# Kernel tuning notes

Hardware: AMD Instinct MI355X
Metric: run time of the kernel (lower is better)

Reference implementation:

```python
import jax, jax.numpy as jnp
import numpy as np

N_NODES = 50000
N_EDGES = 1600000
D_FEAT = 128
ORDER = 2


def setup_inputs() -> dict:
    key = jax.random.key(0)
    k1, k2, k3, k4 = jax.random.split(key, 4)
    x = jax.random.normal(k1, (N_NODES, D_FEAT), dtype=jnp.float32)
    adj_row = jax.random.randint(k2, (N_EDGES,), 0, N_NODES, dtype=jnp.int32)
    adj_col = jax.random.randint(k3, (N_EDGES,), 0, N_NODES, dtype=jnp.int32)
    adj_vals = jax.random.uniform(k4, (N_EDGES,), dtype=jnp.float32)
    return {"x": x, "adj_row": adj_row, "adj_col": adj_col, "adj_vals": adj_vals}


def reference(x, adj_row, adj_col, adj_vals):
    # SGC propagation: x <- A @ x, repeated `order` times.
    # A is sparse COO: A[row, col] = vals; spmm(A, x)[i] = sum_e vals[e]*x[col[e]] into row[e].
    for _ in range(ORDER):
        msgs = adj_vals[:, None] * x[adj_col]          # [E, F] gathered messages
        x = jax.ops.segment_sum(msgs, adj_row, num_segments=N_NODES)  # [N, F]
    return x
```

## Files before the change

kernel.cpp:

```cpp
#include <hip/hip_runtime.h>
#include <hip/hip_fp16.h>

#define N_NODES 50000
#define N_EDGES 1600000
#define D_FEAT  128
#define NB      196
#define BCAP    8704
#define SPAIR_STRIDE (BCAP * 2)
#define S_OUT_CAP 9216
#define OVF_CAP  8192
#define NWAVES  (N_NODES / 2)
#define XWORDS  (N_NODES * (D_FEAT / 2))

#define P1_WGS   400
#define P1_ROUND 4096
#define P1_CAP   38

typedef unsigned u32x2 __attribute__((ext_vector_type(2)));
typedef int      i32x4 __attribute__((ext_vector_type(4)));
typedef float    f32x2 __attribute__((ext_vector_type(2)));
typedef float    f32x4 __attribute__((ext_vector_type(4)));

__device__ __forceinline__ unsigned short f2bf(float f) {
    union { float f; unsigned u; } v; v.f = f;
    unsigned r = v.u + 0x7fff + ((v.u >> 16) & 1);
    return (unsigned short)(r >> 16);
}
__device__ __forceinline__ float bf_lo(unsigned w) {
    union { unsigned u; float f; } v; v.u = w << 16; return v.f;
}
__device__ __forceinline__ float bf_hi(unsigned w) {
    union { unsigned u; float f; } v; v.u = w & 0xffff0000u; return v.f;
}

__global__ __launch_bounds__(256) void p1_bin_kernel(
    const int* __restrict__ row, const int* __restrict__ col,
    const float* __restrict__ val,
    int* __restrict__ gcnt, uint2* __restrict__ sedge, uint2* __restrict__ ovf)
{
    __shared__ uint2    s_buf[NB * P1_CAP];
    __shared__ unsigned s_cnt[NB];
    __shared__ int      s_base[NB];

    int wg = blockIdx.x, t = threadIdx.x;
    int e0 = (int)((long)wg * N_EDGES / P1_WGS);
    int e1 = (int)((long)(wg + 1) * N_EDGES / P1_WGS);

    for (int rbase = e0; rbase < e1; rbase += P1_ROUND) {
        int rend = rbase + P1_ROUND; if (rend > e1) rend = e1;
        for (int i = t; i < NB; i += 256) s_cnt[i] = 0;
        __syncthreads();
        for (int e = rbase + t; e < rend; e += 256) {
            int r = row[e];
            int b = r >> 8;
            uint2 rec;
            rec.x = ((unsigned)r << 16) | (unsigned)col[e];
            rec.y = __float_as_uint(val[e]);
            unsigned pos = atomicAdd(&s_cnt[b], 1u);
            if (pos < P1_CAP) {
                s_buf[b * P1_CAP + pos] = rec;
            } else {
                int p = atomicAdd(&gcnt[b], 1);
                if (p < BCAP) sedge[(long)b * BCAP + p] = rec;
                else {
                    int q = atomicAdd(&gcnt[NB], 1);
                    if (q < OVF_CAP) ovf[q] = rec;
                }
            }
        }
        __syncthreads();
        if (t < NB) {
            int c = (int)s_cnt[t]; if (c > P1_CAP) c = P1_CAP;
            s_base[t] = (c > 0) ? atomicAdd(&gcnt[t], c) : 0;
        }
        __syncthreads();
        if (t < NB) {
            int c = (int)s_cnt[t]; if (c > P1_CAP) c = P1_CAP;
            int gb = s_base[t];
            for (int i = 0; i < c; ++i) {
                int p = gb + i;
                if (p < BCAP) sedge[(long)t * BCAP + p] = s_buf[t * P1_CAP + i];
                else {
                    int q = atomicAdd(&gcnt[NB], 1);
                    if (q < OVF_CAP) ovf[q] = s_buf[t * P1_CAP + i];
                }
            }
        }
        __syncthreads();
    }
}

__global__ __launch_bounds__(1024) void p2_sort_conv_kernel(
    const int* __restrict__ gcnt, const uint2* __restrict__ sedge,
    const uint2* __restrict__ ovf,
    unsigned* __restrict__ spair, int2* __restrict__ row_se,
    const float2* __restrict__ xin, unsigned* __restrict__ xb)
{
    __shared__ unsigned s_out[S_OUT_CAP];
    __shared__ int s_cnt[256];
    __shared__ int s_cur[256];

    int b = blockIdx.x, t = threadIdx.x;
    int cnt = gcnt[b]; if (cnt > BCAP) cnt = BCAP;
    int ovn = gcnt[NB]; if (ovn > OVF_CAP) ovn = OVF_CAP;
    int row0 = b << 8;
    long sbase = (long)b * BCAP;

    if (t < 256) s_cnt[t] = 0;
    __syncthreads();
    for (int i = t; i < cnt; i += 1024) {
        u32x2 rv = __builtin_nontemporal_load((const u32x2*)(sedge + sbase + i));
        int fr = (int)(rv.x >> 16) - row0;
        atomicAdd(&s_cnt[fr], 1);
    }
    for (int i = t; i < ovn; i += 1024) {
        int r = (int)(ovf[i].x >> 16);
        if ((r >> 8) == b) atomicAdd(&s_cnt[r - row0], 1);
    }
    __syncthreads();
    int orig = (t < 256) ? s_cnt[t] : 0;
    __syncthreads();
    for (int off = 1; off < 256; off <<= 1) {
        int u = (t >= off && t < 256) ? s_cnt[t - off] : 0;
        __syncthreads();
        if (t < 256) s_cnt[t] += u;
        __syncthreads();
    }
    int total = s_cnt[255];
    if (t < 256) {
        int excl = s_cnt[t] - orig;
        int r = row0 + t;
        if (r < N_NODES) row_se[r] = make_int2(b * SPAIR_STRIDE + excl, orig);
        s_cur[t] = excl;
    }
    __syncthreads();

    if (total <= S_OUT_CAP) {
        for (int i = t; i < cnt; i += 1024) {
            u32x2 rv = __builtin_nontemporal_load((const u32x2*)(sedge + sbase + i));
            int fr = (int)(rv.x >> 16) - row0;
            int p = atomicAdd(&s_cur[fr], 1);
            unsigned short hv = __half_as_ushort(__float2half(__uint_as_float(rv.y)));
            s_out[p] = ((rv.x & 0xffffu) << 16) | (unsigned)hv;
        }
        for (int i = t; i < ovn; i += 1024) {
            uint2 rec = ovf[i];
            int rr = (int)(rec.x >> 16);
            if ((rr >> 8) == b) {
                int p = atomicAdd(&s_cur[rr - row0], 1);
                unsigned short hv = __half_as_ushort(__float2half(__uint_as_float(rec.y)));
                s_out[p] = ((rec.x & 0xffffu) << 16) | (unsigned)hv;
            }
        }
        __syncthreads();
        for (int i = t; i < total; i += 1024)
            __builtin_nontemporal_store(s_out[i], spair + (long)b * SPAIR_STRIDE + i);
    } else {
        for (int i = t; i < cnt; i += 1024) {
            uint2 rec = sedge[sbase + i];
            int fr = (int)(rec.x >> 16) - row0;
            int p = atomicAdd(&s_cur[fr], 1);
            unsigned short hv = __half_as_ushort(__float2half(__uint_as_float(rec.y)));
            spair[(long)b * SPAIR_STRIDE + p] = ((rec.x & 0xffffu) << 16) | (unsigned)hv;
        }
    }

    for (long g = (long)b * 1024 + t; g < XWORDS; g += (long)NB * 1024) {
        f32x2 f = __builtin_nontemporal_load((const f32x2*)xin + g);
        xb[g] = ((unsigned)f2bf(f.y) << 16) | (unsigned)f2bf(f.x);
    }
}

template <bool WRITE_BF16>
__global__ __launch_bounds__(256) void spmm_csr_bf2_kernel(
    const int2*     __restrict__ row_se,
    const unsigned* __restrict__ spair,
    const unsigned* __restrict__ xb,
    unsigned* __restrict__ outb,
    float*    __restrict__ outf)
{
    int wave = (blockIdx.x * blockDim.x + threadIdx.x) >> 6;
    if (wave >= NWAVES) return;
    int lane = threadIdx.x & 63;
    int half  = lane >> 5;
    int fl    = lane & 31;
    int hbase = lane & 32;
    int row   = wave * 2 + half;

    const i32x4 s4 = __builtin_nontemporal_load((const i32x4*)row_se + wave);
    int mystart = half ? s4.z : s4.x;
    int myn     = half ? s4.w : s4.y;
    int nmax    = (s4.y > s4.w) ? s4.y : s4.w;

    float acc0 = 0.f, acc1 = 0.f, acc2 = 0.f, acc3 = 0.f;

    for (int base = 0; base < nmax; base += 32) {
        int idx = base + fl;
        unsigned rec = 0;
        if (idx < myn) rec = __builtin_nontemporal_load(spair + mystart + idx);
        int   c = (int)(rec >> 16);
        float v = __half2float(__ushort_as_half((unsigned short)(rec & 0xffffu)));

        int steps = nmax - base; if (steps > 32) steps = 32;
        int j = 0;
        for (; j + 8 <= steps; j += 8) {
            int   cc[8];
            float vv[8];
            uint2 ww[8];
            #pragma unroll
            for (int k = 0; k < 8; ++k) {
                cc[k] = __shfl(c, hbase + j + k, 64);
                vv[k] = __shfl(v, hbase + j + k, 64);
            }
            #pragma unroll
            for (int k = 0; k < 8; ++k)
                ww[k] = *(const uint2*)(xb + (long)cc[k] * (D_FEAT / 2) + fl * 2);
            #pragma unroll
            for (int k = 0; k < 8; ++k) {
                acc0 += vv[k] * bf_lo(ww[k].x);
                acc1 += vv[k] * bf_hi(ww[k].x);
                acc2 += vv[k] * bf_lo(ww[k].y);
                acc3 += vv[k] * bf_hi(ww[k].y);
            }
        }
        for (; j < steps; ++j) {
            int   cj = __shfl(c, hbase + j, 64);
            float vj = __shfl(v, hbase + j, 64);
            uint2 w = *(const uint2*)(xb + (long)cj * (D_FEAT / 2) + fl * 2);
            acc0 += vj * bf_lo(w.x);
            acc1 += vj * bf_hi(w.x);
            acc2 += vj * bf_lo(w.y);
            acc3 += vj * bf_hi(w.y);
        }
    }

    if (WRITE_BF16) {
        u32x2 w;
        w.x = ((unsigned)f2bf(acc1) << 16) | (unsigned)f2bf(acc0);
        w.y = ((unsigned)f2bf(acc3) << 16) | (unsigned)f2bf(acc2);
        __builtin_nontemporal_store(w, (u32x2*)(outb + (long)row * (D_FEAT / 2) + fl * 2));
    } else {
        f32x4 w = {acc0, acc1, acc2, acc3};
        __builtin_nontemporal_store(w, (f32x4*)(outf + (long)row * D_FEAT + fl * 4));
    }
}

__global__ __launch_bounds__(256) void spmm_atomic_kernel(
    const int* __restrict__ row, const int* __restrict__ col,
    const float* __restrict__ vals, const float* __restrict__ xin,
    float* __restrict__ xout)
{
    long tid   = (long)blockIdx.x * blockDim.x + threadIdx.x;
    int  edge  = (int)(tid >> 5);
    int  chunk = (int)(tid & 31);
    if (edge >= N_EDGES) return;
    int   r = row[edge];
    int   c = col[edge];
    float v = vals[edge];
    const float4 xv = ((const float4*)(xin + (long)c * D_FEAT))[chunk];
    float* dst = xout + (long)r * D_FEAT + chunk * 4;
    unsafeAtomicAdd(dst + 0, v * xv.x);
    unsafeAtomicAdd(dst + 1, v * xv.y);
    unsafeAtomicAdd(dst + 2, v * xv.z);
    unsafeAtomicAdd(dst + 3, v * xv.w);
}

static inline size_t align_up(size_t x, size_t a) { return (x + a - 1) & ~(a - 1); }

extern "C" void kernel_launch(void* const* d_in, const int* in_sizes, int n_in,
                              void* d_out, int out_size, void* d_ws, size_t ws_size,
                              hipStream_t stream) {
    const float* x        = (const float*)d_in[0];
    const int*   adj_row  = (const int*)d_in[1];
    const int*   adj_col  = (const int*)d_in[2];
    const float* adj_vals = (const float*)d_in[3];
    float*       out      = (float*)d_out;

    const size_t bf_bytes = (size_t)N_NODES * (D_FEAT / 2) * sizeof(unsigned);

    char*     ws      = (char*)d_ws;
    size_t    off     = 0;
    unsigned* xb      = (unsigned*)(ws + off); off = align_up(off + bf_bytes, 512);
    unsigned* tmpb    = (unsigned*)(ws + off); off = align_up(off + bf_bytes, 512);
    uint2*    sedge   = (uint2*)   (ws + off); off = align_up(off + (size_t)NB * BCAP * 8, 512);
    int2*     row_se  = (int2*)    (ws + off); off = align_up(off + (size_t)(NB * 256) * 8, 512);
    int*      gcnt    = (int*)     (ws + off); off = align_up(off + (NB + 1) * sizeof(int), 512);
    uint2*    ovf     = (uint2*)   (ws + off); off = align_up(off + (size_t)OVF_CAP * 8, 512);
    const size_t needed = off;

    unsigned* spair = (unsigned*)sedge;

    const int block = 256;

    if (ws_size >= needed) {
        hipMemsetAsync(gcnt, 0, (NB + 1) * sizeof(int), stream);

        p1_bin_kernel<<<P1_WGS, block, 0, stream>>>(adj_row, adj_col, adj_vals,
                                                    gcnt, sedge, ovf);

        p2_sort_conv_kernel<<<NB, 1024, 0, stream>>>(
            gcnt, sedge, ovf, spair, row_se, (const float2*)x, xb);

        int ngrid = (int)(((long)NWAVES * 64 + block - 1) / block);
        spmm_csr_bf2_kernel<true><<<ngrid, block, 0, stream>>>(
            row_se, spair, xb, tmpb, (float*)nullptr);
        spmm_csr_bf2_kernel<false><<<ngrid, block, 0, stream>>>(
            row_se, spair, tmpb, (unsigned*)nullptr, out);
    } else {
        float* tmp = (float*)ws;
        const size_t feat_bytes = (size_t)N_NODES * D_FEAT * sizeof(float);
        hipMemsetAsync(tmp, 0, feat_bytes, stream);
        hipMemsetAsync(out, 0, feat_bytes, stream);
        long total_threads = (long)N_EDGES * 32;
        long grid = (total_threads + block - 1) / block;
        spmm_atomic_kernel<<<dim3((unsigned)grid), dim3(block), 0, stream>>>(
            adj_row, adj_col, adj_vals, x, tmp);
        spmm_atomic_kernel<<<dim3((unsigned)grid), dim3(block), 0, stream>>>(
            adj_row, adj_col, adj_vals, tmp, out);
    }
}
```

Before: 221.3 us.

## Split feature dimension in halves with four rows per wave in SpMM

Each wave now processes four rows with 16 lanes apiece, covering only one 64-feature half. The two halves are assigned to separate grid halves, which doubles the number of waves. Each gather becomes a 128-byte half-row read, and the shorter 16-edge chunks reduce idle lanes when row lengths are unbalanced. The cost is that every edge record and column index is now read twice, and the accesses to the source feature table become less contiguous.

```diff
diff --git a/kernel.cpp b/kernel.cpp
--- a/kernel.cpp
+++ b/kernel.cpp
@@ -9,15 +9,15 @@
 #define SPAIR_STRIDE (BCAP * 2)
 #define S_OUT_CAP 9216
 #define OVF_CAP  8192
-#define NWAVES  (N_NODES / 2)
 #define XWORDS  (N_NODES * (D_FEAT / 2))
+#define NQWAVES (N_NODES / 4)
 
 #define P1_WGS   400
 #define P1_ROUND 4096
 #define P1_CAP   38
 
 typedef unsigned u32x2 __attribute__((ext_vector_type(2)));
-typedef int      i32x4 __attribute__((ext_vector_type(4)));
+typedef int      i32x2 __attribute__((ext_vector_type(2)));
 typedef float    f32x2 __attribute__((ext_vector_type(2)));
 typedef float    f32x4 __attribute__((ext_vector_type(4)));
 
@@ -172,36 +172,42 @@
 }
 
 template <bool WRITE_BF16>
-__global__ __launch_bounds__(256) void spmm_csr_bf2_kernel(
+__global__ __launch_bounds__(256) void spmm_fh_kernel(
     const int2*     __restrict__ row_se,
     const unsigned* __restrict__ spair,
     const unsigned* __restrict__ xb,
     unsigned* __restrict__ outb,
     float*    __restrict__ outf)
 {
-    int wave = (blockIdx.x * blockDim.x + threadIdx.x) >> 6;
-    if (wave >= NWAVES) return;
-    int lane = threadIdx.x & 63;
-    int half  = lane >> 5;
-    int fl    = lane & 31;
-    int hbase = lane & 32;
-    int row   = wave * 2 + half;
-
-    const i32x4 s4 = __builtin_nontemporal_load((const i32x4*)row_se + wave);
-    int mystart = half ? s4.z : s4.x;
-    int myn     = half ? s4.w : s4.y;
-    int nmax    = (s4.y > s4.w) ? s4.y : s4.w;
+    int gw = (blockIdx.x * blockDim.x + threadIdx.x) >> 6;
+    if (gw >= 2 * NQWAVES) return;
+    int lane  = threadIdx.x & 63;
+    int half  = (gw >= NQWAVES) ? 1 : 0;
+    int wq    = gw - half * NQWAVES;
+    int q     = lane >> 4;
+    int fl    = lane & 15;
+    int qbase = lane & 48;
+    int row   = wq * 4 + q;
+
+    i32x2 se = __builtin_nontemporal_load((const i32x2*)row_se + row);
+    int mystart = se.x;
+    int myn     = se.y;
+    int nmax = myn;
+    nmax = max(nmax, __shfl_xor(nmax, 16, 64));
+    nmax = max(nmax, __shfl_xor(nmax, 32, 64));
+
+    const unsigned* xbh = xb + half * 32;
 
     float acc0 = 0.f, acc1 = 0.f, acc2 = 0.f, acc3 = 0.f;
 
-    for (int base = 0; base < nmax; base += 32) {
+    for (int base = 0; base < nmax; base += 16) {
         int idx = base + fl;
         unsigned rec = 0;
         if (idx < myn) rec = __builtin_nontemporal_load(spair + mystart + idx);
         int   c = (int)(rec >> 16);
         float v = __half2float(__ushort_as_half((unsigned short)(rec & 0xffffu)));
 
-        int steps = nmax - base; if (steps > 32) steps = 32;
+        int steps = nmax - base; if (steps > 16) steps = 16;
         int j = 0;
         for (; j + 8 <= steps; j += 8) {
             int   cc[8];
@@ -209,12 +215,12 @@
             uint2 ww[8];
             #pragma unroll
             for (int k = 0; k < 8; ++k) {
-                cc[k] = __shfl(c, hbase + j + k, 64);
-                vv[k] = __shfl(v, hbase + j + k, 64);
+                cc[k] = __shfl(c, qbase + j + k, 64);
+                vv[k] = __shfl(v, qbase + j + k, 64);
             }
             #pragma unroll
             for (int k = 0; k < 8; ++k)
-                ww[k] = *(const uint2*)(xb + (long)cc[k] * (D_FEAT / 2) + fl * 2);
+                ww[k] = *(const uint2*)(xbh + (long)cc[k] * (D_FEAT / 2) + fl * 2);
             #pragma unroll
             for (int k = 0; k < 8; ++k) {
                 acc0 += vv[k] * bf_lo(ww[k].x);
@@ -224,9 +230,9 @@
             }
         }
         for (; j < steps; ++j) {
-            int   cj = __shfl(c, hbase + j, 64);
-            float vj = __shfl(v, hbase + j, 64);
-            uint2 w = *(const uint2*)(xb + (long)cj * (D_FEAT / 2) + fl * 2);
+            int   cj = __shfl(c, qbase + j, 64);
+            float vj = __shfl(v, qbase + j, 64);
+            uint2 w = *(const uint2*)(xbh + (long)cj * (D_FEAT / 2) + fl * 2);
             acc0 += vj * bf_lo(w.x);
             acc1 += vj * bf_hi(w.x);
             acc2 += vj * bf_lo(w.y);
@@ -238,10 +244,12 @@
         u32x2 w;
         w.x = ((unsigned)f2bf(acc1) << 16) | (unsigned)f2bf(acc0);
         w.y = ((unsigned)f2bf(acc3) << 16) | (unsigned)f2bf(acc2);
-        __builtin_nontemporal_store(w, (u32x2*)(outb + (long)row * (D_FEAT / 2) + fl * 2));
+        __builtin_nontemporal_store(w,
+            (u32x2*)(outb + (long)row * (D_FEAT / 2) + half * 32 + fl * 2));
     } else {
         f32x4 w = {acc0, acc1, acc2, acc3};
-        __builtin_nontemporal_store(w, (f32x4*)(outf + (long)row * D_FEAT + fl * 4));
+        __builtin_nontemporal_store(w,
+            (f32x4*)(outf + (long)row * D_FEAT + half * 64 + fl * 4));
     }
 }
 
@@ -301,10 +309,10 @@
         p2_sort_conv_kernel<<<NB, 1024, 0, stream>>>(
             gcnt, sedge, ovf, spair, row_se, (const float2*)x, xb);
 
-        int ngrid = (int)(((long)NWAVES * 64 + block - 1) / block);
-        spmm_csr_bf2_kernel<true><<<ngrid, block, 0, stream>>>(
+        int ngrid = (int)(((long)2 * NQWAVES * 64 + block - 1) / block);
+        spmm_fh_kernel<true><<<ngrid, block, 0, stream>>>(
             row_se, spair, xb, tmpb, (float*)nullptr);
-        spmm_csr_bf2_kernel<false><<<ngrid, block, 0, stream>>>(
+        spmm_fh_kernel<false><<<ngrid, block, 0, stream>>>(
             row_se, spair, tmpb, (unsigned*)nullptr, out);
     } else {
         float* tmp = (float*)ws;
```

New measurement: 219.5 us. About the same (-0.8%).
